# Kernel optimization log

Measured on AMD Instinct MI355X. Metric: run time of the kernel, lower is better.

## Reference

```python
import jax, jax.numpy as jnp
import numpy as np

THETA = 10000.0
NUM_HEADS = 16


def _rope(x, pos, theta):
    # x: [..., T, d_k], pos: [T]
    d_k = x.shape[-1]
    inv_freq = 1.0 / theta ** (jnp.arange(0, d_k, 2, dtype=jnp.float32) / d_k)
    ang = pos.astype(jnp.float32)[:, None] * inv_freq  # [T, d_k/2]
    cos, sin = jnp.cos(ang), jnp.sin(ang)
    x1, x2 = x[..., ::2], x[..., 1::2]
    even = x1 * cos - x2 * sin
    odd = x1 * sin + x2 * cos
    return jnp.stack([even, odd], axis=-1).reshape(x.shape)


def setup_inputs() -> dict:
    key = jax.random.key(0)
    ks = jax.random.split(key, 5)
    B, T, D = 4, 2048, 1024
    return {
        "in_features": jax.random.normal(ks[0], (B, T, D), dtype=jnp.float32),
        "token_positions": jnp.arange(T, dtype=jnp.int64 if jax.config.jax_enable_x64 else jnp.int32),
        "Wq": jax.random.normal(ks[1], (D, D), dtype=jnp.float32) * 0.02,
        "Wk": jax.random.normal(ks[2], (D, D), dtype=jnp.float32) * 0.02,
        "Wv": jax.random.normal(ks[3], (D, D), dtype=jnp.float32) * 0.02,
        "Wo": jax.random.normal(ks[4], (D, D), dtype=jnp.float32) * 0.02,
    }


def reference(in_features, token_positions, Wq, Wk, Wv, Wo):
    B, T, D = in_features.shape
    h = NUM_HEADS
    d_k = D // h
    # projections (weight stored [out, in], torch applies x @ W.T)
    Q = in_features @ Wq.T
    K = in_features @ Wk.T
    V = in_features @ Wv.T
    # [B, T, h*d_k] -> [B, h, T, d_k]
    Q = Q.reshape(B, T, h, d_k).transpose(0, 2, 1, 3)
    K = K.reshape(B, T, h, d_k).transpose(0, 2, 1, 3)
    V = V.reshape(B, T, h, d_k).transpose(0, 2, 1, 3)
    Q = _rope(Q, token_positions, THETA)
    K = _rope(K, token_positions, THETA)
    scores = jnp.einsum("bhqd,bhkd->bhqk", Q, K) / jnp.sqrt(jnp.float32(d_k))
    causal = jnp.tril(jnp.ones((T, T), dtype=bool))
    scores = jnp.where(causal, scores, -jnp.inf)
    attn = jax.nn.softmax(scores, axis=-1)
    heads = jnp.einsum("bhqk,bhkd->bhqd", attn, V)
    out = heads.transpose(0, 2, 1, 3).reshape(B, T, D)
    return out @ Wo.T
```

## Files before the change

kernel.cpp:

```cpp
#include <hip/hip_runtime.h>


typedef unsigned short u16;
typedef short short8 __attribute__((ext_vector_type(8)));
typedef float f32x4 __attribute__((ext_vector_type(4)));

#if defined(__has_builtin)
#if __has_builtin(__builtin_amdgcn_exp2f)
#define EXP2(x) __builtin_amdgcn_exp2f(x)
#else
#define EXP2(x) exp2f(x)
#endif
#else
#define EXP2(x) exp2f(x)
#endif

__device__ __forceinline__ float bf2f(u16 u) {
  return __uint_as_float(((unsigned int)u) << 16);
}
__device__ __forceinline__ u16 f2bf(float f) {
  unsigned int x = __float_as_uint(f);
  x += 0x7fff + ((x >> 16) & 1);
  return (u16)(x >> 16);
}

__device__ __forceinline__ void glds16(const u16* g, u16* l) {
  __builtin_amdgcn_global_load_lds(
      (const __attribute__((address_space(1))) unsigned int*)g,
      (__attribute__((address_space(3))) unsigned int*)l, 16, 0, 0);
}

__global__ __launch_bounds__(256) void cvt_bf16(const float* __restrict__ in,
                                                u16* __restrict__ out) {
  const int i = (blockIdx.x * 256 + threadIdx.x) * 8;
  const float4 a = *(const float4*)(in + i);
  const float4 b = *(const float4*)(in + i + 4);
  short8 o;
  o[0] = (short)f2bf(a.x); o[1] = (short)f2bf(a.y);
  o[2] = (short)f2bf(a.z); o[3] = (short)f2bf(a.w);
  o[4] = (short)f2bf(b.x); o[5] = (short)f2bf(b.y);
  o[6] = (short)f2bf(b.z); o[7] = (short)f2bf(b.w);
  *(short8*)(out + i) = o;
}

__global__ __launch_bounds__(256) void gemm_qkv(const u16* __restrict__ A,
                                                const u16* __restrict__ W,
                                                u16* __restrict__ Qd,
                                                u16* __restrict__ Kd,
                                                u16* __restrict__ Vd) {
  const int K = 1024;
  __shared__ __align__(16) u16 As[128 * 32];
  __shared__ __align__(16) u16 Bs[128 * 32];
  const int tid = threadIdx.x;
  const int m0 = blockIdx.y << 7;
  const int n0 = blockIdx.x << 7;
  const int w = tid >> 6, L = tid & 63;
  const int wm = (w >> 1) << 6, wn = (w & 1) << 6;
  const int lane15 = L & 15, quad = L >> 4;
  const int koff = quad << 3;

  f32x4 acc[4][4] = {};

  const int s0 = tid, s1 = tid + 256;
  const int r0 = s0 >> 2, c0 = (s0 & 3) << 3;
  const int r1 = s1 >> 2, c1 = (s1 & 3) << 3;
  const u16* A0 = A + (size_t)(m0 + r0) * K + c0;
  const u16* A1 = A + (size_t)(m0 + r1) * K + c1;
  const u16* B0 = W + (size_t)(n0 + r0) * K + c0;
  const u16* B1 = W + (size_t)(n0 + r1) * K + c1;
  u16* asd0 = &As[s0 * 8]; u16* asd1 = &As[s1 * 8];
  u16* bsd0 = &Bs[s0 * 8]; u16* bsd1 = &Bs[s1 * 8];

  for (int k0 = 0; k0 < K; k0 += 32) {
    __syncthreads();
    glds16(A0 + k0, asd0);
    glds16(A1 + k0, asd1);
    glds16(B0 + k0, bsd0);
    glds16(B1 + k0, bsd1);
    __syncthreads();
    short8 a[4], b[4];
#pragma unroll
    for (int mt = 0; mt < 4; ++mt)
      a[mt] = *(const short8*)&As[(wm + mt * 16 + lane15) * 32 + koff];
#pragma unroll
    for (int nt = 0; nt < 4; ++nt)
      b[nt] = *(const short8*)&Bs[(wn + nt * 16 + lane15) * 32 + koff];
#pragma unroll
    for (int mt = 0; mt < 4; ++mt)
#pragma unroll
      for (int nt = 0; nt < 4; ++nt)
        acc[mt][nt] =
            __builtin_amdgcn_mfma_f32_16x16x32_bf16(a[mt], b[nt], acc[mt][nt], 0, 0, 0);
  }

  u16* dst = (n0 < 1024) ? Qd : (n0 < 2048 ? Kd : Vd);
  const int ncol0 = (n0 & 1023) + wn;
#pragma unroll
  for (int mt = 0; mt < 4; ++mt) {
    const int rbase = m0 + wm + mt * 16 + (quad << 2);
#pragma unroll
    for (int nt = 0; nt < 4; ++nt) {
      const int col = ncol0 + nt * 16 + lane15;
#pragma unroll
      for (int r = 0; r < 4; ++r)
        dst[(size_t)(rbase + r) * 1024 + col] = f2bf(acc[mt][nt][r]);
    }
  }
}

__global__ __launch_bounds__(256) void gemm_bt(const u16* __restrict__ A,
                                               const u16* __restrict__ B,
                                               float* __restrict__ C,
                                               int M, int N, int K) {
  __shared__ __align__(16) u16 As[128 * 32];
  __shared__ __align__(16) u16 Bs[128 * 32];
  const int tid = threadIdx.x;
  const int m0 = blockIdx.y << 7;
  const int n0 = blockIdx.x << 7;
  const int w = tid >> 6, L = tid & 63;
  const int wm = (w >> 1) << 6, wn = (w & 1) << 6;
  const int lane15 = L & 15, quad = L >> 4;
  const int koff = quad << 3;

  f32x4 acc[4][4] = {};

  const int s0 = tid, s1 = tid + 256;
  const int r0 = s0 >> 2, c0 = (s0 & 3) << 3;
  const int r1 = s1 >> 2, c1 = (s1 & 3) << 3;
  const u16* A0 = A + (size_t)(m0 + r0) * K + c0;
  const u16* A1 = A + (size_t)(m0 + r1) * K + c1;
  const u16* B0 = B + (size_t)(n0 + r0) * K + c0;
  const u16* B1 = B + (size_t)(n0 + r1) * K + c1;
  u16* asd0 = &As[s0 * 8]; u16* asd1 = &As[s1 * 8];
  u16* bsd0 = &Bs[s0 * 8]; u16* bsd1 = &Bs[s1 * 8];

  for (int k0 = 0; k0 < K; k0 += 32) {
    __syncthreads();
    glds16(A0 + k0, asd0);
    glds16(A1 + k0, asd1);
    glds16(B0 + k0, bsd0);
    glds16(B1 + k0, bsd1);
    __syncthreads();
    short8 a[4], b[4];
#pragma unroll
    for (int mt = 0; mt < 4; ++mt)
      a[mt] = *(const short8*)&As[(wm + mt * 16 + lane15) * 32 + koff];
#pragma unroll
    for (int nt = 0; nt < 4; ++nt)
      b[nt] = *(const short8*)&Bs[(wn + nt * 16 + lane15) * 32 + koff];
#pragma unroll
    for (int mt = 0; mt < 4; ++mt)
#pragma unroll
      for (int nt = 0; nt < 4; ++nt)
        acc[mt][nt] =
            __builtin_amdgcn_mfma_f32_16x16x32_bf16(a[mt], b[nt], acc[mt][nt], 0, 0, 0);
  }

#pragma unroll
  for (int mt = 0; mt < 4; ++mt) {
    const int rbase = m0 + wm + mt * 16 + (quad << 2);
#pragma unroll
    for (int nt = 0; nt < 4; ++nt) {
      const int col = n0 + wn + nt * 16 + lane15;
#pragma unroll
      for (int r = 0; r < 4; ++r)
        C[(size_t)(rbase + r) * N + col] = acc[mt][nt][r];
    }
  }
}

__global__ __launch_bounds__(256) void rope_table(const int* __restrict__ pos,
                                                  float2* __restrict__ tab) {
  const int gid = blockIdx.x * 256 + threadIdx.x;
  const int d2 = gid & 31;
  const int t = gid >> 5;
  double inv = pow(10000.0, -(double)d2 / 32.0);
  double ang = (double)pos[t] * inv;
  tab[gid] = make_float2((float)cos(ang), (float)sin(ang));
}

__global__ __launch_bounds__(256) void rope_qk(const u16* __restrict__ in,
                                               const float2* __restrict__ tab,
                                               u16* __restrict__ out, float scale) {
  const int gid = blockIdx.x * 256 + threadIdx.x;
  const int d2 = gid & 31;
  const int h = (gid >> 5) & 15;
  const int t = (gid >> 9) & 2047;
  const int b = gid >> 20;
  const unsigned int v =
      *(const unsigned int*)(in + (((size_t)(b * 2048 + t)) << 10) + (h << 6) + (d2 << 1));
  const float x1 = bf2f((u16)(v & 0xffff));
  const float x2 = bf2f((u16)(v >> 16));
  const float2 cs = tab[(t << 5) + d2];
  const float e = (x1 * cs.x - x2 * cs.y) * scale;
  const float o = (x1 * cs.y + x2 * cs.x) * scale;
  const unsigned int ov = (unsigned int)f2bf(e) | ((unsigned int)f2bf(o) << 16);
  *(unsigned int*)(out + (((size_t)((b * 16 + h) * 2048 + t)) << 6) + (d2 << 1)) = ov;
}

__global__ __launch_bounds__(256) void transpose_v(const u16* __restrict__ Vlin,
                                                   u16* __restrict__ Vt) {
  __shared__ __align__(16) u16 tile[64][68];
  const int tid = threadIdx.x;
  const int bh = blockIdx.y, b = bh >> 4, h = bh & 15;
  const int t0 = blockIdx.x << 6;
#pragma unroll
  for (int i = 0; i < 4; ++i) {
    int s = tid + (i << 8);
    int tl = s >> 4, c4 = (s & 15) << 2;
    *(uint2*)&tile[tl][c4] =
        *(const uint2*)(Vlin + (((size_t)(b * 2048 + t0 + tl)) << 10) + (h << 6) + c4);
  }
  __syncthreads();
#pragma unroll
  for (int i = 0; i < 4; ++i) {
    int s = tid + (i << 8);
    int d = s >> 4, t4 = (s & 15) << 2;
    uint2 o;
    o.x = (unsigned)tile[t4 + 0][d] | ((unsigned)tile[t4 + 1][d] << 16);
    o.y = (unsigned)tile[t4 + 2][d] | ((unsigned)tile[t4 + 3][d] << 16);
    *(uint2*)(Vt + (((size_t)(bh * 64 + d)) << 11) + t0 + t4) = o;
  }
}

__global__ __launch_bounds__(256) void flash_attn(const u16* __restrict__ Q,
                                                  const u16* __restrict__ Kk,
                                                  const u16* __restrict__ Vt,
                                                  u16* __restrict__ O) {
  __shared__ __align__(16) u16 Ksm[2][64 * 72];
  __shared__ __align__(16) u16 Vsm[2][64 * 72];
  __shared__ __align__(16) u16 Psm[4][16 * 64];
  const int tid = threadIdx.x;
  const int w = tid >> 6, L = tid & 63;
  const int lane15 = L & 15, quad = L >> 4;
  const int qt = 15 - (blockIdx.x >> 6);
  const int bh = blockIdx.x & 63;
  const int b = bh >> 4, h = bh & 15;
  const int rq = lane15 >> 2;
  const int nkt = 2 * qt + 2;

  const int s0 = tid, s1 = tid + 256;
  const u16* kbase = Kk + ((size_t)bh << 17);
  const u16* kp0 = kbase + s0 * 8;
  const u16* kp1 = kbase + s1 * 8;
  const u16* vbase = Vt + ((size_t)bh << 17);
  const u16* vp0 = vbase + (size_t)(s0 >> 3) * 2048 + (s0 & 7) * 8;
  const u16* vp1 = vbase + (size_t)(s1 >> 3) * 2048 + (s1 & 7) * 8;
  const int d0 = (s0 >> 3) * 72 + (s0 & 7) * 8;
  const int d1 = (s1 >> 3) * 72 + (s1 & 7) * 8;
  u16* pw = Psm[w];

  const size_t qrow = (size_t)bh * 2048 + qt * 128 + w * 32;
  short8 qa[2][2];
#pragma unroll
  for (int hf = 0; hf < 2; ++hf) {
    const size_t qb = (qrow + hf * 16 + lane15) << 6;
    qa[hf][0] = *(const short8*)(Q + qb + (quad << 3));
    qa[hf][1] = *(const short8*)(Q + qb + 32 + (quad << 3));
  }

  uint4 kr0 = *(const uint4*)kp0;
  uint4 kr1 = *(const uint4*)kp1;
  uint4 vr0 = *(const uint4*)vp0;
  uint4 vr1 = *(const uint4*)vp1;
  *(uint4*)&Ksm[0][d0] = kr0; *(uint4*)&Ksm[0][d1] = kr1;
  *(uint4*)&Vsm[0][d0] = vr0; *(uint4*)&Vsm[0][d1] = vr1;
  __syncthreads();

  f32x4 o_acc[2][4] = {};
  float l_part[2][4] = {};

  for (int kt = 0; kt < nkt; ++kt) {
    const int cur = kt & 1, nxt = cur ^ 1;
    if (kt + 1 < nkt) {
      kr0 = *(const uint4*)(kp0 + (size_t)(kt + 1) * 4096);
      kr1 = *(const uint4*)(kp1 + (size_t)(kt + 1) * 4096);
      vr0 = *(const uint4*)(vp0 + (kt + 1) * 64);
      vr1 = *(const uint4*)(vp1 + (kt + 1) * 64);
    }
    const u16* Ks = Ksm[cur];
    const u16* Vs = Vsm[cur];

    short8 kb[4][2];
#pragma unroll
    for (int nt = 0; nt < 4; ++nt) {
      kb[nt][0] = *(const short8*)&Ks[(nt * 16 + lane15) * 72 + (quad << 3)];
      kb[nt][1] = *(const short8*)&Ks[(nt * 16 + lane15) * 72 + 32 + (quad << 3)];
    }

#pragma unroll
    for (int hf = 0; hf < 2; ++hf) {
      const int B0 = qt * 128 + w * 32 + hf * 16;
      if (kt * 64 > B0 + 15) continue;

      f32x4 sc[4];
#pragma unroll
      for (int nt = 0; nt < 4; ++nt) {
        f32x4 a = {};
        a = __builtin_amdgcn_mfma_f32_16x16x32_bf16(qa[hf][0], kb[nt][0], a, 0, 0, 0);
        a = __builtin_amdgcn_mfma_f32_16x16x32_bf16(qa[hf][1], kb[nt][1], a, 0, 0, 0);
        sc[nt] = a;
      }

      if (kt * 64 + 63 > B0) {
#pragma unroll
        for (int nt = 0; nt < 4; ++nt)
#pragma unroll
          for (int r = 0; r < 4; ++r) {
            const int row = B0 + (quad << 2) + r;
            const int key = kt * 64 + nt * 16 + lane15;
            if (key > row) sc[nt][r] = -1e30f;
          }
      }

      asm volatile("" ::: "memory");
#pragma unroll
      for (int nt = 0; nt < 4; ++nt) {
        const int colsw = ((nt ^ quad) << 4) + lane15;
#pragma unroll
        for (int r = 0; r < 4; ++r) {
          const float p = EXP2(sc[nt][r]);
          l_part[hf][r] += p;
          const unsigned int u = __float_as_uint(p) + 0x8000u;
          pw[((quad << 2) + r) * 64 + colsw] = (u16)(u >> 16);
        }
      }
      asm volatile("" ::: "memory");

#pragma unroll
      for (int ks = 0; ks < 2; ++ks) {
        const short8 pa =
            *(const short8*)&pw[lane15 * 64 + ((ks * 32 + quad * 8) ^ (rq << 4))];
#pragma unroll
        for (int dt = 0; dt < 4; ++dt) {
          const short8 vb =
              *(const short8*)&Vs[(dt * 16 + lane15) * 72 + ks * 32 + quad * 8];
          o_acc[hf][dt] =
              __builtin_amdgcn_mfma_f32_16x16x32_bf16(pa, vb, o_acc[hf][dt], 0, 0, 0);
        }
      }
    }

    if (kt + 1 < nkt) {
      *(uint4*)&Ksm[nxt][d0] = kr0; *(uint4*)&Ksm[nxt][d1] = kr1;
      *(uint4*)&Vsm[nxt][d0] = vr0; *(uint4*)&Vsm[nxt][d1] = vr1;
    }
    __syncthreads();
  }

#pragma unroll
  for (int hf = 0; hf < 2; ++hf) {
#pragma unroll
    for (int r = 0; r < 4; ++r) {
      float l = l_part[hf][r];
#pragma unroll
      for (int off = 1; off < 16; off <<= 1) l += __shfl_xor(l, off, 64);
      const float inv = 1.f / l;
      const int t = qt * 128 + w * 32 + hf * 16 + (quad << 2) + r;
      const size_t obase = (((size_t)b * 2048 + t) << 10) + (h << 6);
#pragma unroll
      for (int dt = 0; dt < 4; ++dt)
        O[obase + dt * 16 + lane15] = f2bf(o_acc[hf][dt][r] * inv);
    }
  }
}

extern "C" void kernel_launch(void* const* d_in, const int* in_sizes, int n_in,
                              void* d_out, int out_size, void* d_ws, size_t ws_size,
                              hipStream_t stream) {
  const float* X  = (const float*)d_in[0];
  const int* pos  = (const int*)d_in[1];
  const float* Wq = (const float*)d_in[2];
  const float* Wk = (const float*)d_in[3];
  const float* Wv = (const float*)d_in[4];
  const float* Wo = (const float*)d_in[5];
  float* out = (float*)d_out;

  char* ws = (char*)d_ws;
  const size_t SZ = (size_t)8192 * 1024 * sizeof(u16);
  const size_t WSZ = (size_t)1024 * 1024 * sizeof(u16);
  u16* Qlin = (u16*)(ws + 0 * SZ);
  u16* Klin = (u16*)(ws + 1 * SZ);
  u16* Vlin = (u16*)(ws + 2 * SZ);
  u16* Qr   = (u16*)(ws + 3 * SZ);
  u16* Kr   = (u16*)(ws + 4 * SZ);
  u16* Vt   = (u16*)(ws + 5 * SZ);
  u16* Xb   = (u16*)(ws + 6 * SZ);
  u16* Oh   = Qlin;
  char* wtail = ws + 7 * SZ;
  u16* Wqkvb = (u16*)(wtail);
  u16* Wob   = (u16*)(wtail + 3 * WSZ);
  float2* tab = (float2*)(wtail + 4 * WSZ);

  const dim3 blk(256);

  cvt_bf16<<<4096, blk, 0, stream>>>(X, Xb);
  cvt_bf16<<<512, blk, 0, stream>>>(Wq, Wqkvb);
  cvt_bf16<<<512, blk, 0, stream>>>(Wk, Wqkvb + 1024 * 1024);
  cvt_bf16<<<512, blk, 0, stream>>>(Wv, Wqkvb + 2 * 1024 * 1024);
  cvt_bf16<<<512, blk, 0, stream>>>(Wo, Wob);
  rope_table<<<256, blk, 0, stream>>>(pos, tab);
  gemm_qkv<<<dim3(24, 64), blk, 0, stream>>>(Xb, Wqkvb, Qlin, Klin, Vlin);
  rope_qk<<<16384, blk, 0, stream>>>(Qlin, tab, Qr, 0.18033688011112042f);
  rope_qk<<<16384, blk, 0, stream>>>(Klin, tab, Kr, 1.0f);
  transpose_v<<<dim3(32, 64), blk, 0, stream>>>(Vlin, Vt);
  flash_attn<<<1024, blk, 0, stream>>>(Qr, Kr, Vt, Oh);
  gemm_bt<<<dim3(8, 64), blk, 0, stream>>>(Oh, Wob, out, 8192, 1024, 1024);
}
```

Before: 294.2 us.

## Fuse RoPE into QKV GEMM epilogue and single-buffer flash-attention K/V tiles

Applies RoPE and the Q scale directly in the QKV GEMM epilogue, using a lane shuffle to pair even and odd columns, and writes head-major Q/K. This removes the two separate rope_qk launches and their round trip through global memory. Flash attention drops from double-buffered to single-buffered K/V shared memory with an extra barrier per tile, and gives each half-tile its own P buffer. The bf16 conversion of P now truncates instead of rounding, which slightly changes precision. The epilogue now does scattered 2-byte stores into the head-major layout, and the extra barrier in attention may expose load latency.

```diff
diff --git a/kernel.cpp b/kernel.cpp
--- a/kernel.cpp
+++ b/kernel.cpp
@@ -14,6 +14,8 @@
 #else
 #define EXP2(x) exp2f(x)
 #endif
+
+#define QSCALE 0.18033688011112042f
 
 __device__ __forceinline__ float bf2f(u16 u) {
   return __uint_as_float(((unsigned int)u) << 16);
@@ -45,8 +47,9 @@
 
 __global__ __launch_bounds__(256) void gemm_qkv(const u16* __restrict__ A,
                                                 const u16* __restrict__ W,
-                                                u16* __restrict__ Qd,
-                                                u16* __restrict__ Kd,
+                                                const float2* __restrict__ tab,
+                                                u16* __restrict__ Qr,
+                                                u16* __restrict__ Kr,
                                                 u16* __restrict__ Vd) {
   const int K = 1024;
   __shared__ __align__(16) u16 As[128 * 32];
@@ -93,17 +96,42 @@
             __builtin_amdgcn_mfma_f32_16x16x32_bf16(a[mt], b[nt], acc[mt][nt], 0, 0, 0);
   }
 
-  u16* dst = (n0 < 1024) ? Qd : (n0 < 2048 ? Kd : Vd);
+  const int sel = n0 >> 10;
   const int ncol0 = (n0 & 1023) + wn;
-#pragma unroll
-  for (int mt = 0; mt < 4; ++mt) {
-    const int rbase = m0 + wm + mt * 16 + (quad << 2);
-#pragma unroll
-    for (int nt = 0; nt < 4; ++nt) {
-      const int col = ncol0 + nt * 16 + lane15;
-#pragma unroll
-      for (int r = 0; r < 4; ++r)
-        dst[(size_t)(rbase + r) * 1024 + col] = f2bf(acc[mt][nt][r]);
+  if (sel == 2) {
+#pragma unroll
+    for (int mt = 0; mt < 4; ++mt) {
+      const int rbase = m0 + wm + mt * 16 + (quad << 2);
+#pragma unroll
+      for (int nt = 0; nt < 4; ++nt) {
+        const int col = ncol0 + nt * 16 + lane15;
+#pragma unroll
+        for (int r = 0; r < 4; ++r)
+          Vd[(size_t)(rbase + r) * 1024 + col] = f2bf(acc[mt][nt][r]);
+      }
+    }
+  } else {
+    u16* dst = sel ? Kr : Qr;
+    const float sc = sel ? 1.0f : QSCALE;
+#pragma unroll
+    for (int mt = 0; mt < 4; ++mt) {
+      const int rbase = m0 + wm + mt * 16 + (quad << 2);
+#pragma unroll
+      for (int nt = 0; nt < 4; ++nt) {
+        const int col = ncol0 + nt * 16 + lane15;
+        const int h = col >> 6, dcol = col & 63, d2 = dcol >> 1;
+#pragma unroll
+        for (int r = 0; r < 4; ++r) {
+          const int m = rbase + r;
+          const int bb = m >> 11, tt = m & 2047;
+          const float2 cs = tab[(tt << 5) + d2];
+          const float self = acc[mt][nt][r];
+          const float part = __shfl_xor(self, 1, 64);
+          const float res = (dcol & 1) ? (part * cs.y + self * cs.x)
+                                       : (self * cs.x - part * cs.y);
+          dst[(((size_t)((bb * 16 + h) * 2048 + tt)) << 6) + dcol] = f2bf(res * sc);
+        }
+      }
     }
   }
 }
@@ -179,25 +207,6 @@
   tab[gid] = make_float2((float)cos(ang), (float)sin(ang));
 }
 
-__global__ __launch_bounds__(256) void rope_qk(const u16* __restrict__ in,
-                                               const float2* __restrict__ tab,
-                                               u16* __restrict__ out, float scale) {
-  const int gid = blockIdx.x * 256 + threadIdx.x;
-  const int d2 = gid & 31;
-  const int h = (gid >> 5) & 15;
-  const int t = (gid >> 9) & 2047;
-  const int b = gid >> 20;
-  const unsigned int v =
-      *(const unsigned int*)(in + (((size_t)(b * 2048 + t)) << 10) + (h << 6) + (d2 << 1));
-  const float x1 = bf2f((u16)(v & 0xffff));
-  const float x2 = bf2f((u16)(v >> 16));
-  const float2 cs = tab[(t << 5) + d2];
-  const float e = (x1 * cs.x - x2 * cs.y) * scale;
-  const float o = (x1 * cs.y + x2 * cs.x) * scale;
-  const unsigned int ov = (unsigned int)f2bf(e) | ((unsigned int)f2bf(o) << 16);
-  *(unsigned int*)(out + (((size_t)((b * 16 + h) * 2048 + t)) << 6) + (d2 << 1)) = ov;
-}
-
 __global__ __launch_bounds__(256) void transpose_v(const u16* __restrict__ Vlin,
                                                    u16* __restrict__ Vt) {
   __shared__ __align__(16) u16 tile[64][68];
@@ -227,9 +236,9 @@
                                                   const u16* __restrict__ Kk,
                                                   const u16* __restrict__ Vt,
                                                   u16* __restrict__ O) {
-  __shared__ __align__(16) u16 Ksm[2][64 * 72];
-  __shared__ __align__(16) u16 Vsm[2][64 * 72];
-  __shared__ __align__(16) u16 Psm[4][16 * 64];
+  __shared__ __align__(16) u16 Ksm[64 * 72];
+  __shared__ __align__(16) u16 Vsm[64 * 72];
+  __shared__ __align__(16) u16 Psm[8][16 * 64];
   const int tid = threadIdx.x;
   const int w = tid >> 6, L = tid & 63;
   const int lane15 = L & 15, quad = L >> 4;
@@ -248,7 +257,6 @@
   const u16* vp1 = vbase + (size_t)(s1 >> 3) * 2048 + (s1 & 7) * 8;
   const int d0 = (s0 >> 3) * 72 + (s0 & 7) * 8;
   const int d1 = (s1 >> 3) * 72 + (s1 & 7) * 8;
-  u16* pw = Psm[w];
 
   const size_t qrow = (size_t)bh * 2048 + qt * 128 + w * 32;
   short8 qa[2][2];
@@ -263,35 +271,33 @@
   uint4 kr1 = *(const uint4*)kp1;
   uint4 vr0 = *(const uint4*)vp0;
   uint4 vr1 = *(const uint4*)vp1;
-  *(uint4*)&Ksm[0][d0] = kr0; *(uint4*)&Ksm[0][d1] = kr1;
-  *(uint4*)&Vsm[0][d0] = vr0; *(uint4*)&Vsm[0][d1] = vr1;
+  *(uint4*)&Ksm[d0] = kr0; *(uint4*)&Ksm[d1] = kr1;
+  *(uint4*)&Vsm[d0] = vr0; *(uint4*)&Vsm[d1] = vr1;
   __syncthreads();
 
   f32x4 o_acc[2][4] = {};
   float l_part[2][4] = {};
 
   for (int kt = 0; kt < nkt; ++kt) {
-    const int cur = kt & 1, nxt = cur ^ 1;
     if (kt + 1 < nkt) {
       kr0 = *(const uint4*)(kp0 + (size_t)(kt + 1) * 4096);
       kr1 = *(const uint4*)(kp1 + (size_t)(kt + 1) * 4096);
       vr0 = *(const uint4*)(vp0 + (kt + 1) * 64);
       vr1 = *(const uint4*)(vp1 + (kt + 1) * 64);
     }
-    const u16* Ks = Ksm[cur];
-    const u16* Vs = Vsm[cur];
 
     short8 kb[4][2];
 #pragma unroll
     for (int nt = 0; nt < 4; ++nt) {
-      kb[nt][0] = *(const short8*)&Ks[(nt * 16 + lane15) * 72 + (quad << 3)];
-      kb[nt][1] = *(const short8*)&Ks[(nt * 16 + lane15) * 72 + 32 + (quad << 3)];
+      kb[nt][0] = *(const short8*)&Ksm[(nt * 16 + lane15) * 72 + (quad << 3)];
+      kb[nt][1] = *(const short8*)&Ksm[(nt * 16 + lane15) * 72 + 32 + (quad << 3)];
     }
 
 #pragma unroll
     for (int hf = 0; hf < 2; ++hf) {
       const int B0 = qt * 128 + w * 32 + hf * 16;
       if (kt * 64 > B0 + 15) continue;
+      u16* pw = Psm[w * 2 + hf];
 
       f32x4 sc[4];
 #pragma unroll
@@ -321,8 +327,7 @@
         for (int r = 0; r < 4; ++r) {
           const float p = EXP2(sc[nt][r]);
           l_part[hf][r] += p;
-          const unsigned int u = __float_as_uint(p) + 0x8000u;
-          pw[((quad << 2) + r) * 64 + colsw] = (u16)(u >> 16);
+          pw[((quad << 2) + r) * 64 + colsw] = (u16)(__float_as_uint(p) >> 16);
         }
       }
       asm volatile("" ::: "memory");
@@ -334,7 +339,7 @@
 #pragma unroll
         for (int dt = 0; dt < 4; ++dt) {
           const short8 vb =
-              *(const short8*)&Vs[(dt * 16 + lane15) * 72 + ks * 32 + quad * 8];
+              *(const short8*)&Vsm[(dt * 16 + lane15) * 72 + ks * 32 + quad * 8];
           o_acc[hf][dt] =
               __builtin_amdgcn_mfma_f32_16x16x32_bf16(pa, vb, o_acc[hf][dt], 0, 0, 0);
         }
@@ -342,10 +347,11 @@
     }
 
     if (kt + 1 < nkt) {
-      *(uint4*)&Ksm[nxt][d0] = kr0; *(uint4*)&Ksm[nxt][d1] = kr1;
-      *(uint4*)&Vsm[nxt][d0] = vr0; *(uint4*)&Vsm[nxt][d1] = vr1;
-    }
-    __syncthreads();
+      __syncthreads();
+      *(uint4*)&Ksm[d0] = kr0; *(uint4*)&Ksm[d1] = kr1;
+      *(uint4*)&Vsm[d0] = vr0; *(uint4*)&Vsm[d1] = vr1;
+      __syncthreads();
+    }
   }
 
 #pragma unroll
@@ -379,15 +385,13 @@
   char* ws = (char*)d_ws;
   const size_t SZ = (size_t)8192 * 1024 * sizeof(u16);
   const size_t WSZ = (size_t)1024 * 1024 * sizeof(u16);
-  u16* Qlin = (u16*)(ws + 0 * SZ);
-  u16* Klin = (u16*)(ws + 1 * SZ);
-  u16* Vlin = (u16*)(ws + 2 * SZ);
-  u16* Qr   = (u16*)(ws + 3 * SZ);
-  u16* Kr   = (u16*)(ws + 4 * SZ);
-  u16* Vt   = (u16*)(ws + 5 * SZ);
-  u16* Xb   = (u16*)(ws + 6 * SZ);
-  u16* Oh   = Qlin;
-  char* wtail = ws + 7 * SZ;
+  u16* Vlin = (u16*)(ws + 0 * SZ);
+  u16* Qr   = (u16*)(ws + 1 * SZ);
+  u16* Kr   = (u16*)(ws + 2 * SZ);
+  u16* Vt   = (u16*)(ws + 3 * SZ);
+  u16* Xb   = (u16*)(ws + 4 * SZ);
+  u16* Oh   = Vlin;
+  char* wtail = ws + 5 * SZ;
   u16* Wqkvb = (u16*)(wtail);
   u16* Wob   = (u16*)(wtail + 3 * WSZ);
   float2* tab = (float2*)(wtail + 4 * WSZ);
@@ -400,9 +404,7 @@
   cvt_bf16<<<512, blk, 0, stream>>>(Wv, Wqkvb + 2 * 1024 * 1024);
   cvt_bf16<<<512, blk, 0, stream>>>(Wo, Wob);
   rope_table<<<256, blk, 0, stream>>>(pos, tab);
-  gemm_qkv<<<dim3(24, 64), blk, 0, stream>>>(Xb, Wqkvb, Qlin, Klin, Vlin);
-  rope_qk<<<16384, blk, 0, stream>>>(Qlin, tab, Qr, 0.18033688011112042f);
-  rope_qk<<<16384, blk, 0, stream>>>(Klin, tab, Kr, 1.0f);
+  gemm_qkv<<<dim3(24, 64), blk, 0, stream>>>(Xb, Wqkvb, tab, Qr, Kr, Vlin);
   transpose_v<<<dim3(32, 64), blk, 0, stream>>>(Vlin, Vt);
   flash_attn<<<1024, blk, 0, stream>>>(Qr, Kr, Vt, Oh);
   gemm_bt<<<dim3(8, 64), blk, 0, stream>>>(Oh, Wob, out, 8192, 1024, 1024);
```

New measurement: 296.4 us. No clear change (+0.8%).
